# Performance work log

Hardware: AMD Instinct MI355X
Metric: run time of the kernel (lower is better)

## Reference

```python
import jax, jax.numpy as jnp
import numpy as np

V, D, H, L, B, S = 8192, 128, 8, 2, 1, 128
HD = D // H
HID = int(8 * D / 3)
EPS = 1e-6


def setup_inputs() -> dict:
    key = jax.random.key(0)
    ks = jax.random.split(key, 12)
    sc = 0.02
    return {
        "idx": jax.random.randint(ks[0], (B, S), 0, V),
        "w_raw": jax.random.normal(ks[1], (D, V), jnp.float32) * sc,
        "norm1_w": jnp.ones((L, D), jnp.float32),
        "norm2_w": jnp.ones((L, D), jnp.float32),
        "wq": jax.random.normal(ks[2], (L, D, D), jnp.float32) * sc,
        "wk": jax.random.normal(ks[3], (L, D, D), jnp.float32) * sc,
        "wv": jax.random.normal(ks[4], (L, D, D), jnp.float32) * sc,
        "wo": jax.random.normal(ks[5], (L, D, D), jnp.float32) * sc,
        "w1": jax.random.normal(ks[6], (L, D, HID), jnp.float32) * sc,
        "w3": jax.random.normal(ks[7], (L, D, HID), jnp.float32) * sc,
        "w2": jax.random.normal(ks[8], (L, HID, D), jnp.float32) * sc,
        "final_norm_w": jnp.ones((D,), jnp.float32),
    }


def rmsnorm(x, w):
    return x * jax.lax.rsqrt(jnp.mean(x * x, axis=-1, keepdims=True) + EPS) * w


def rope_cos_sin(seqlen, hd):
    inv = 1.0 / (10000.0 ** (jnp.arange(0, hd, 2, dtype=jnp.float32) / hd))
    t = jnp.arange(seqlen, dtype=jnp.float32)
    f = jnp.outer(t, inv)  # (S, hd/2)
    return jnp.cos(f), jnp.sin(f)


def apply_rope(x, cos, sin):
    # x: (B,S,H,HD); interleaved complex pairs as in Llama
    x0, x1 = x[..., 0::2], x[..., 1::2]
    c = cos[None, :, None, :]
    s = sin[None, :, None, :]
    r0 = x0 * c - x1 * s
    r1 = x0 * s + x1 * c
    return jnp.stack([r0, r1], axis=-1).reshape(x.shape)


def forward(idx, w_raw, norm1_w, norm2_w, wq, wk, wv, wo, w1, w2, w3, final_norm_w):
    Wemb = jax.nn.sigmoid(w_raw)                 # (D,V)
    x = Wemb.T[idx]                              # Yoneda one-hot @ W.T == gather -> (B,S,D)
    cos, sin = rope_cos_sin(S, HD)
    causal = jnp.tril(jnp.ones((S, S), bool))[None, None]  # (1,1,S,S)
    scale = 1.0 / jnp.sqrt(jnp.float32(HD))
    for i in range(L):
        # Multi-Universe attention (heads == universes), RoPE, causal SDPA
        h = rmsnorm(x, norm1_w[i])
        q = (h @ wq[i]).reshape(B, S, H, HD)
        k = (h @ wk[i]).reshape(B, S, H, HD)
        v = (h @ wv[i]).reshape(B, S, H, HD)
        q = apply_rope(q, cos, sin)
        k = apply_rope(k, cos, sin)
        scores = jnp.einsum("bihd,bjhd->bhij", q, k) * scale
        scores = jnp.where(causal, scores, jnp.float32(-1e9))
        attn = jax.nn.softmax(scores, axis=-1)
        o = jnp.einsum("bhij,bjhd->bihd", attn, v).reshape(B, S, D) @ wo[i]
        x = x + o
        # SwiGLU FFN
        h2 = rmsnorm(x, norm2_w[i])
        x = x + (jax.nn.silu(h2 @ w1[i]) * (h2 @ w3[i])) @ w2[i]
    x_norm = rmsnorm(x, final_norm_w)
    # Godel-Heyting reachability head
    x_n = x_norm / jnp.linalg.norm(x_norm, axis=-1, keepdims=True)      # (B,S,D)
    v_n = (Wemb / jnp.linalg.norm(Wemb, axis=0, keepdims=True)).T        # (V,D)
    a = x_n[:, :, None, :]                                               # (B,S,1,D)
    b = v_n[None, None, :, :]                                            # (1,1,V,D)
    # strict Godel implication: a => b = 1 if a <= b else b
    imp = jnp.where(a <= b, jnp.float32(1.0), b)                         # (B,S,V,D)
    logits = jnp.clip(imp.mean(axis=-1), 1e-6, 1.0 - 1e-6)               # (B,S,V)
    return logits


def reference(idx, w_raw, norm1_w, norm2_w, wq, wk, wv, wo, w1, w2, w3, final_norm_w):
    return forward(idx, w_raw, norm1_w, norm2_w, wq, wk, wv, wo, w1, w2, w3, final_norm_w)
```

## Files before the change

### kernel.cpp

```cpp
#include <hip/hip_runtime.h>
#include <math.h>

#define V 8192
#define D 128
#define NH 8
#define HD 16
#define SEQ 128
#define HID 341
#define EPS 1e-6f

__device__ __forceinline__ float sigm(float x) { return 1.0f / (1.0f + __expf(-x)); }

__device__ __forceinline__ float block_sum256(float v, float* scratch) {
    #pragma unroll
    for (int m = 32; m > 0; m >>= 1) v += __shfl_xor(v, m);
    if ((threadIdx.x & 63) == 0) scratch[threadIdx.x >> 6] = v;
    __syncthreads();
    float s = (scratch[0] + scratch[1]) + (scratch[2] + scratch[3]);
    __syncthreads();
    return s;
}

__device__ __forceinline__ float block_sum512(float v, float* scratch) {
    #pragma unroll
    for (int m = 32; m > 0; m >>= 1) v += __shfl_xor(v, m);
    if ((threadIdx.x & 63) == 0) scratch[threadIdx.x >> 6] = v;
    __syncthreads();
    float s = ((scratch[0] + scratch[1]) + (scratch[2] + scratch[3])) +
              ((scratch[4] + scratch[5]) + (scratch[6] + scratch[7]));
    __syncthreads();
    return s;
}

__global__ __launch_bounds__(256, 1) void k_embed_qkv(
    const int* __restrict__ idx, const float* __restrict__ w_raw,
    const float* __restrict__ wq, const float* __restrict__ wk,
    const float* __restrict__ wv, const float* __restrict__ n1w,
    const float* __restrict__ w1, const float* __restrict__ w3,
    const float* __restrict__ w2, const float* __restrict__ wo,
    float* __restrict__ x, float* __restrict__ q, float* __restrict__ k,
    float* __restrict__ v, float* __restrict__ sink) {
    int t = threadIdx.x;
    if (blockIdx.x >= SEQ) {
        int g = (blockIdx.x - SEQ) * 256 + t;
        float acc = 0.f;
        const float4* p = (const float4*)w_raw;
        for (int i = g; i < 262144; i += 65536) {
            float4 u = p[i];
            acc += u.x + u.y + u.z + u.w;
        }
        p = (const float4*)w1;
        if (g < 21824) { float4 u = p[g]; acc += u.x + u.y + u.z + u.w; }
        p = (const float4*)w3;
        if (g < 21824) { float4 u = p[g]; acc += u.x + u.y + u.z + u.w; }
        p = (const float4*)w2;
        if (g < 21824) { float4 u = p[g]; acc += u.x + u.y + u.z + u.w; }
        p = (const float4*)wq;
        if (g < 8192) { float4 u = p[g]; acc += u.x + u.y + u.z + u.w; }
        p = (const float4*)wk;
        if (g < 8192) { float4 u = p[g]; acc += u.x + u.y + u.z + u.w; }
        p = (const float4*)wv;
        if (g < 8192) { float4 u = p[g]; acc += u.x + u.y + u.z + u.w; }
        p = (const float4*)wo;
        if (g < 8192) { float4 u = p[g]; acc += u.x + u.y + u.z + u.w; }
        if (acc == 1234.5678f) sink[0] = acc;
        return;
    }
    __shared__ float hr[D], qrow[D], krow[D], vpart[2][D], scr[4];
    int s = blockIdx.x;
    int col = t & 127, half = t >> 7, dlo = half * 64;
    float xv = 0.f;
    if (t < 128) xv = sigm(w_raw[t * V + idx[s]]);
    float wpre[128];
    const float* wsel = (t < 128) ? wq : wk;
    #pragma unroll
    for (int d = 0; d < 128; ++d) wpre[d] = wsel[d * D + col];
    float wvpre[64];
    #pragma unroll
    for (int d = 0; d < 64; ++d) wvpre[d] = wv[(dlo + d) * D + col];
    if (t < 128) x[s * D + t] = xv;
    float ss = block_sum256(xv * xv, scr);
    float r = 1.0f / sqrtf(ss * (1.0f / D) + EPS);
    if (t < 128) hr[t] = xv * r * n1w[t];
    __syncthreads();
    float a0 = 0, a1 = 0, a2 = 0, a3 = 0;
    #pragma unroll
    for (int d = 0; d < 128; d += 4) {
        a0 += hr[d] * wpre[d];
        a1 += hr[d + 1] * wpre[d + 1];
        a2 += hr[d + 2] * wpre[d + 2];
        a3 += hr[d + 3] * wpre[d + 3];
    }
    float qk = (a0 + a1) + (a2 + a3);
    float b0 = 0, b1 = 0, b2 = 0, b3 = 0;
    #pragma unroll
    for (int d = 0; d < 64; d += 4) {
        b0 += hr[dlo + d] * wvpre[d];
        b1 += hr[dlo + d + 1] * wvpre[d + 1];
        b2 += hr[dlo + d + 2] * wvpre[d + 2];
        b3 += hr[dlo + d + 3] * wvpre[d + 3];
    }
    vpart[half][col] = (b0 + b1) + (b2 + b3);
    if (t < 128) qrow[col] = qk;
    else krow[col] = qk;
    __syncthreads();
    if (t < 128) {
        v[s * D + t] = vpart[0][t] + vpart[1][t];
        int c = t & (HD - 1);
        int m = c >> 1;
        float fr = (float)s * expf(-(float)m * 1.15129254649702283e+00f);
        float cs = cosf(fr), sn = sinf(fr);
        int base = t & ~1;
        float qe = qrow[base], qod = qrow[base + 1];
        float ke = krow[base], kod = krow[base + 1];
        q[s * D + t] = (c & 1) ? (qe * sn + qod * cs) : (qe * cs - qod * sn);
        k[s * D + t] = (c & 1) ? (ke * sn + kod * cs) : (ke * cs - kod * sn);
    }
}

template <int MODE>
__global__ __launch_bounds__(512, 2) void k_layer(
    const float* __restrict__ q, const float* __restrict__ kg,
    const float* __restrict__ vg, float* __restrict__ x,
    const float* __restrict__ wo, const float* __restrict__ n2w,
    const float* __restrict__ w1, const float* __restrict__ w3,
    const float* __restrict__ w2, const float* __restrict__ wq,
    const float* __restrict__ wk, const float* __restrict__ wv,
    const float* __restrict__ n1w, float* __restrict__ qo, float* __restrict__ ko,
    float* __restrict__ vo, const float* __restrict__ fw, float* __restrict__ xng) {
    __shared__ float ps[NH][SEQ + 1];
    __shared__ float qs[D], orow[D], h2[D];
    __shared__ float part[4][D];
    __shared__ float afA[HID], afB[HID], af[HID];
    __shared__ float rl[NH];
    __shared__ float scr[8];
    int s = blockIdx.x, t = threadIdx.x;
    int col = t & 127, quarter = t >> 7;
    int jlo = quarter * 32, dlo = quarter * 32;

    float qv = 0.f, xr = 0.f;
    if (t < 128) {
        qv = q[s * D + t];
        xr = x[s * D + t];
    }
    float4 kp[2][4];
    #pragma unroll
    for (int u = 0; u < 2; ++u) {
        const float4* p = (const float4*)&kg[col * D + (quarter + 4 * u) * HD];
        kp[u][0] = p[0]; kp[u][1] = p[1]; kp[u][2] = p[2]; kp[u][3] = p[3];
    }
    float vpre[32];
    #pragma unroll
    for (int j = 0; j < 32; ++j) vpre[j] = vg[(jlo + j) * D + col];
    float wopre[32];
    #pragma unroll
    for (int u = 0; u < 32; ++u) wopre[u] = wo[(dlo + u) * D + col];

    if (t < 128) qs[t] = qv;
    __syncthreads();

    #pragma unroll
    for (int u = 0; u < 2; ++u) {
        int h = quarter + 4 * u;
        const float* qh = &qs[h * HD];
        float acc = kp[u][0].x * qh[0] + kp[u][0].y * qh[1] + kp[u][0].z * qh[2] +
                    kp[u][0].w * qh[3] + kp[u][1].x * qh[4] + kp[u][1].y * qh[5] +
                    kp[u][1].z * qh[6] + kp[u][1].w * qh[7] + kp[u][2].x * qh[8] +
                    kp[u][2].y * qh[9] + kp[u][2].z * qh[10] + kp[u][2].w * qh[11] +
                    kp[u][3].x * qh[12] + kp[u][3].y * qh[13] + kp[u][3].z * qh[14] +
                    kp[u][3].w * qh[15];
        ps[h][col] = (col <= s) ? acc * 0.25f : 0.f;
    }
    __syncthreads();

    {
        int h = t >> 6, lane = t & 63;
        float pm = -1e30f;
        for (int j = lane; j <= s; j += 64) pm = fmaxf(pm, ps[h][j]);
        #pragma unroll
        for (int m = 32; m > 0; m >>= 1) pm = fmaxf(pm, __shfl_xor(pm, m));
        float psum = 0.f;
        for (int j = lane; j <= s; j += 64) {
            float e = __expf(ps[h][j] - pm);
            ps[h][j] = e;
            psum += e;
        }
        #pragma unroll
        for (int m = 32; m > 0; m >>= 1) psum += __shfl_xor(psum, m);
        if (lane == 0) rl[h] = 1.0f / psum;
    }
    __syncthreads();

    {
        int h = col >> 4;
        float a0 = 0, a1 = 0, a2 = 0, a3 = 0;
        #pragma unroll
        for (int j = 0; j < 32; j += 4) {
            a0 += ps[h][jlo + j] * vpre[j];
            a1 += ps[h][jlo + j + 1] * vpre[j + 1];
            a2 += ps[h][jlo + j + 2] * vpre[j + 2];
            a3 += ps[h][jlo + j + 3] * vpre[j + 3];
        }
        part[quarter][col] = (a0 + a1) + (a2 + a3);
    }
    __syncthreads();
    if (t < 128) orow[t] = ((part[0][t] + part[1][t]) + (part[2][t] + part[3][t])) * rl[t >> 4];
    __syncthreads();

    {
        float a0 = 0, a1 = 0;
        #pragma unroll
        for (int u = 0; u < 32; u += 2) {
            a0 += orow[dlo + u] * wopre[u];
            a1 += orow[dlo + u + 1] * wopre[u + 1];
        }
        part[quarter][col] = a0 + a1;
    }
    __syncthreads();
    float xn = 0.f;
    if (t < 128) xn = xr + (part[0][t] + part[1][t]) + (part[2][t] + part[3][t]);
    float ss2 = block_sum512((t < 128) ? xn * xn : 0.f, scr);
    float r2 = 1.0f / sqrtf(ss2 * (1.0f / D) + EPS);
    if (t < 128) h2[t] = xn * r2 * n2w[t];
    __syncthreads();

    for (int task = t; task < 2 * HID; task += 512) {
        int mat = task >= HID;
        int c2 = mat ? (task - HID) : task;
        const float* w = mat ? w3 : w1;
        float a0 = 0, a1 = 0, a2 = 0, a3 = 0;
        #pragma unroll 8
        for (int d = 0; d < D; d += 4) {
            a0 += h2[d] * w[d * HID + c2];
            a1 += h2[d + 1] * w[(d + 1) * HID + c2];
            a2 += h2[d + 2] * w[(d + 2) * HID + c2];
            a3 += h2[d + 3] * w[(d + 3) * HID + c2];
        }
        if (mat) afB[c2] = (a0 + a1) + (a2 + a3);
        else afA[c2] = (a0 + a1) + (a2 + a3);
    }
    __syncthreads();
    if (t < HID) {
        float a1v = afA[t];
        af[t] = (a1v / (1.0f + __expf(-a1v))) * afB[t];
    }
    __syncthreads();

    {
        int lo = quarter * 85;
        int hi = (quarter == 3) ? 341 : lo + 85;
        float a0 = 0, a1 = 0, a2 = 0, a3 = 0;
        int tt = lo;
        #pragma unroll 8
        for (; tt + 3 < hi; tt += 4) {
            a0 += af[tt] * w2[tt * D + col];
            a1 += af[tt + 1] * w2[(tt + 1) * D + col];
            a2 += af[tt + 2] * w2[(tt + 2) * D + col];
            a3 += af[tt + 3] * w2[(tt + 3) * D + col];
        }
        for (; tt < hi; ++tt) a0 += af[tt] * w2[tt * D + col];
        part[quarter][col] = (a0 + a1) + (a2 + a3);
    }
    __syncthreads();
    float x2 = 0.f;
    if (t < 128) {
        x2 = xn + (part[0][t] + part[1][t]) + (part[2][t] + part[3][t]);
        if (MODE == 0) x[s * D + t] = x2;
    }

    float ss = block_sum512((t < 128) ? x2 * x2 : 0.f, scr);
    float r = 1.0f / sqrtf(ss * (1.0f / D) + EPS);

    if constexpr (MODE == 0) {
        if (t < 128) h2[t] = x2 * r * n1w[t];
        __syncthreads();
        float qk = 0.f;
        if (quarter < 3) {
            const float* wsel = (quarter == 0) ? wq : ((quarter == 1) ? wk : wv);
            float a0 = 0, a1 = 0, a2 = 0, a3 = 0;
            #pragma unroll 8
            for (int d = 0; d < D; d += 4) {
                a0 += h2[d] * wsel[d * D + col];
                a1 += h2[d + 1] * wsel[(d + 1) * D + col];
                a2 += h2[d + 2] * wsel[(d + 2) * D + col];
                a3 += h2[d + 3] * wsel[(d + 3) * D + col];
            }
            qk = (a0 + a1) + (a2 + a3);
        }
        if (quarter == 0) qs[col] = qk;
        else if (quarter == 1) orow[col] = qk;
        else if (quarter == 2) part[0][col] = qk;
        __syncthreads();
        if (t < 128) {
            vo[s * D + t] = part[0][t];
            int c = t & (HD - 1);
            int mm = c >> 1;
            float fr = (float)s * expf(-(float)mm * 1.15129254649702283e+00f);
            float cs = cosf(fr), sn = sinf(fr);
            int base = t & ~1;
            float qe = qs[base], qod = qs[base + 1];
            float ke = orow[base], kod = orow[base + 1];
            qo[s * D + t] = (c & 1) ? (qe * sn + qod * cs) : (qe * cs - qod * sn);
            ko[s * D + t] = (c & 1) ? (ke * sn + kod * cs) : (ke * cs - kod * sn);
        }
    } else {
        float y = (t < 128) ? x2 * r * fw[t] : 0.f;
        float nn = block_sum512(y * y, scr);
        if (t < 128) xng[t * SEQ + s] = y / sqrtf(nn);
    }
}

__global__ __launch_bounds__(256) void k_logits(const float* __restrict__ xng,
                                                const float* __restrict__ w_raw,
                                                float* __restrict__ out) {
    __shared__ float xs[D * 64];
    __shared__ float vs[D * 32];
    __shared__ float nred[256];
    __shared__ float invn_s[32];
    int t = threadIdx.x;
    int sbase = (blockIdx.x & 1) * 64;
    int vbase = (blockIdx.x >> 1) * 32;
    for (int i = t; i < D * 64; i += 256) {
        int d = i >> 6, s2 = i & 63;
        xs[i] = xng[d * SEQ + sbase + s2];
    }
    for (int i = t; i < D * 32; i += 256) {
        int d = i >> 5, jj = i & 31;
        vs[i] = sigm(w_raw[d * V + vbase + jj]);
    }
    __syncthreads();
    {
        int colc = t & 31, dp = t >> 5;
        float p = 0.f;
        for (int u = 0; u < 16; ++u) {
            float vv = vs[(dp * 16 + u) * 32 + colc];
            p += vv * vv;
        }
        nred[t] = p;
    }
    __syncthreads();
    if (t < 32) {
        float sum = 0.f;
        for (int u = 0; u < 8; ++u) sum += nred[u * 32 + t];
        invn_s[t] = 1.0f / sqrtf(sum);
    }
    __syncthreads();
    for (int i = t; i < D * 32; i += 256) vs[i] *= invn_s[i & 31];
    __syncthreads();
    int vg = t & 15;
    int sg = t >> 4;
    float acc[4][2] = {};
    for (int d = 0; d < D; ++d) {
        float4 xq = *(const float4*)&xs[d * 64 + sg * 4];
        float2 vq = *(const float2*)&vs[d * 32 + vg * 2];
        acc[0][0] += (xq.x <= vq.x) ? 1.0f : vq.x;
        acc[0][1] += (xq.x <= vq.y) ? 1.0f : vq.y;
        acc[1][0] += (xq.y <= vq.x) ? 1.0f : vq.x;
        acc[1][1] += (xq.y <= vq.y) ? 1.0f : vq.y;
        acc[2][0] += (xq.z <= vq.x) ? 1.0f : vq.x;
        acc[2][1] += (xq.z <= vq.y) ? 1.0f : vq.y;
        acc[3][0] += (xq.w <= vq.x) ? 1.0f : vq.x;
        acc[3][1] += (xq.w <= vq.y) ? 1.0f : vq.y;
    }
    const float inv128 = 1.0f / 128.0f;
    #pragma unroll
    for (int si = 0; si < 4; ++si) {
        int s = sbase + sg * 4 + si;
        float2 ov;
        ov.x = fminf(fmaxf(acc[si][0] * inv128, 1e-6f), 1.0f - 1e-6f);
        ov.y = fminf(fmaxf(acc[si][1] * inv128, 1e-6f), 1.0f - 1e-6f);
        *(float2*)&out[s * V + vbase + vg * 2] = ov;
    }
}

extern "C" void kernel_launch(void* const* d_in, const int* in_sizes, int n_in,
                              void* d_out, int out_size, void* d_ws, size_t ws_size,
                              hipStream_t stream) {
    const int* idx = (const int*)d_in[0];
    const float* w_raw = (const float*)d_in[1];
    const float* n1w = (const float*)d_in[2];
    const float* n2w = (const float*)d_in[3];
    const float* wq = (const float*)d_in[4];
    const float* wk = (const float*)d_in[5];
    const float* wv = (const float*)d_in[6];
    const float* wo = (const float*)d_in[7];
    const float* w1 = (const float*)d_in[8];
    const float* w3 = (const float*)d_in[9];
    const float* w2 = (const float*)d_in[10];
    const float* fnw = (const float*)d_in[11];
    float* out = (float*)d_out;
    float* ws = (float*)d_ws;

    float* x    = ws;
    float* q1   = ws + 16384;
    float* k1   = ws + 32768;
    float* v1   = ws + 49152;
    float* q2   = ws + 65536;
    float* k2   = ws + 81920;
    float* v2   = ws + 98304;
    float* xng  = ws + 114688;
    float* sink = ws + 131072;

    k_embed_qkv<<<dim3(SEQ + 256), dim3(256), 0, stream>>>(
        idx, w_raw, wq, wk, wv, n1w, w1, w3, w2, wo, x, q1, k1, v1, sink);
    k_layer<0><<<dim3(SEQ), dim3(512), 0, stream>>>(
        q1, k1, v1, x, wo, n2w, w1, w3, w2,
        wq + D * D, wk + D * D, wv + D * D, n1w + D, q2, k2, v2,
        (const float*)nullptr, (float*)nullptr);
    k_layer<1><<<dim3(SEQ), dim3(512), 0, stream>>>(
        q2, k2, v2, x, wo + D * D, n2w + D, w1 + D * HID, w3 + D * HID,
        w2 + HID * D, (const float*)nullptr, (const float*)nullptr,
        (const float*)nullptr, (const float*)nullptr, (float*)nullptr,
        (float*)nullptr, (float*)nullptr, fnw, xng);
    k_logits<<<dim3(512), dim3(256), 0, stream>>>(xng, w_raw, out);
}
```

Baseline: 141.5 us.

## Widen per-token layer kernel to 1024 threads and drop register prefetch

Doubles the k_layer block from 512 to 1024 threads, so each 128-thread group handles 16 rows instead of 32 for the attention value, output projection and w2 reductions, and one head per group for QK scores. The register prefetch arrays for K, V and Wo are removed; those loads now happen inline inside the loops. The w1/w3 projection becomes a single pass with one task per thread. This aims to cut per-thread serial work and register pressure in a 128-block launch that leaves most CUs idle, at the cost of more partial-sum reduction and of no longer issuing the global loads early.

```diff
diff --git a/kernel.cpp b/kernel.cpp
--- a/kernel.cpp
+++ b/kernel.cpp
@@ -21,13 +21,15 @@
     return s;
 }
 
-__device__ __forceinline__ float block_sum512(float v, float* scratch) {
+__device__ __forceinline__ float block_sum1024(float v, float* scratch) {
     #pragma unroll
     for (int m = 32; m > 0; m >>= 1) v += __shfl_xor(v, m);
     if ((threadIdx.x & 63) == 0) scratch[threadIdx.x >> 6] = v;
     __syncthreads();
     float s = ((scratch[0] + scratch[1]) + (scratch[2] + scratch[3])) +
-              ((scratch[4] + scratch[5]) + (scratch[6] + scratch[7]));
+              ((scratch[4] + scratch[5]) + (scratch[6] + scratch[7])) +
+              ((scratch[8] + scratch[9]) + (scratch[10] + scratch[11])) +
+              ((scratch[12] + scratch[13]) + (scratch[14] + scratch[15]));
     __syncthreads();
     return s;
 }
@@ -119,7 +121,7 @@
 }
 
 template <int MODE>
-__global__ __launch_bounds__(512, 2) void k_layer(
+__global__ __launch_bounds__(1024, 4) void k_layer(
     const float* __restrict__ q, const float* __restrict__ kg,
     const float* __restrict__ vg, float* __restrict__ x,
     const float* __restrict__ wo, const float* __restrict__ n2w,
@@ -130,50 +132,35 @@
     float* __restrict__ vo, const float* __restrict__ fw, float* __restrict__ xng) {
     __shared__ float ps[NH][SEQ + 1];
     __shared__ float qs[D], orow[D], h2[D];
-    __shared__ float part[4][D];
+    __shared__ float part[8][D];
     __shared__ float afA[HID], afB[HID], af[HID];
     __shared__ float rl[NH];
-    __shared__ float scr[8];
+    __shared__ float scr[16];
     int s = blockIdx.x, t = threadIdx.x;
-    int col = t & 127, quarter = t >> 7;
-    int jlo = quarter * 32, dlo = quarter * 32;
+    int col = t & 127, g8 = t >> 7;
+    int jlo = g8 * 16, dlo = g8 * 16;
 
     float qv = 0.f, xr = 0.f;
     if (t < 128) {
         qv = q[s * D + t];
         xr = x[s * D + t];
-    }
-    float4 kp[2][4];
-    #pragma unroll
-    for (int u = 0; u < 2; ++u) {
-        const float4* p = (const float4*)&kg[col * D + (quarter + 4 * u) * HD];
-        kp[u][0] = p[0]; kp[u][1] = p[1]; kp[u][2] = p[2]; kp[u][3] = p[3];
-    }
-    float vpre[32];
-    #pragma unroll
-    for (int j = 0; j < 32; ++j) vpre[j] = vg[(jlo + j) * D + col];
-    float wopre[32];
-    #pragma unroll
-    for (int u = 0; u < 32; ++u) wopre[u] = wo[(dlo + u) * D + col];
-
-    if (t < 128) qs[t] = qv;
-    __syncthreads();
-
-    #pragma unroll
-    for (int u = 0; u < 2; ++u) {
-        int h = quarter + 4 * u;
-        const float* qh = &qs[h * HD];
-        float acc = kp[u][0].x * qh[0] + kp[u][0].y * qh[1] + kp[u][0].z * qh[2] +
-                    kp[u][0].w * qh[3] + kp[u][1].x * qh[4] + kp[u][1].y * qh[5] +
-                    kp[u][1].z * qh[6] + kp[u][1].w * qh[7] + kp[u][2].x * qh[8] +
-                    kp[u][2].y * qh[9] + kp[u][2].z * qh[10] + kp[u][2].w * qh[11] +
-                    kp[u][3].x * qh[12] + kp[u][3].y * qh[13] + kp[u][3].z * qh[14] +
-                    kp[u][3].w * qh[15];
-        ps[h][col] = (col <= s) ? acc * 0.25f : 0.f;
+        qs[t] = qv;
     }
     __syncthreads();
 
     {
+        const float4* kp = (const float4*)&kg[col * D + g8 * HD];
+        float4 k0 = kp[0], k1v = kp[1], k2v = kp[2], k3v = kp[3];
+        const float* qh = &qs[g8 * HD];
+        float acc = k0.x * qh[0] + k0.y * qh[1] + k0.z * qh[2] + k0.w * qh[3] +
+                    k1v.x * qh[4] + k1v.y * qh[5] + k1v.z * qh[6] + k1v.w * qh[7] +
+                    k2v.x * qh[8] + k2v.y * qh[9] + k2v.z * qh[10] + k2v.w * qh[11] +
+                    k3v.x * qh[12] + k3v.y * qh[13] + k3v.z * qh[14] + k3v.w * qh[15];
+        ps[g8][col] = (col <= s) ? acc * 0.25f : 0.f;
+    }
+    __syncthreads();
+
+    if (t < 512) {
         int h = t >> 6, lane = t & 63;
         float pm = -1e30f;
         for (int j = lane; j <= s; j += 64) pm = fmaxf(pm, ps[h][j]);
@@ -195,38 +182,42 @@
         int h = col >> 4;
         float a0 = 0, a1 = 0, a2 = 0, a3 = 0;
         #pragma unroll
-        for (int j = 0; j < 32; j += 4) {
-            a0 += ps[h][jlo + j] * vpre[j];
-            a1 += ps[h][jlo + j + 1] * vpre[j + 1];
-            a2 += ps[h][jlo + j + 2] * vpre[j + 2];
-            a3 += ps[h][jlo + j + 3] * vpre[j + 3];
-        }
-        part[quarter][col] = (a0 + a1) + (a2 + a3);
-    }
-    __syncthreads();
-    if (t < 128) orow[t] = ((part[0][t] + part[1][t]) + (part[2][t] + part[3][t])) * rl[t >> 4];
+        for (int j = 0; j < 16; j += 4) {
+            a0 += ps[h][jlo + j] * vg[(jlo + j) * D + col];
+            a1 += ps[h][jlo + j + 1] * vg[(jlo + j + 1) * D + col];
+            a2 += ps[h][jlo + j + 2] * vg[(jlo + j + 2) * D + col];
+            a3 += ps[h][jlo + j + 3] * vg[(jlo + j + 3) * D + col];
+        }
+        part[g8][col] = (a0 + a1) + (a2 + a3);
+    }
+    __syncthreads();
+    if (t < 128)
+        orow[t] = (((part[0][t] + part[1][t]) + (part[2][t] + part[3][t])) +
+                   ((part[4][t] + part[5][t]) + (part[6][t] + part[7][t]))) * rl[t >> 4];
     __syncthreads();
 
     {
         float a0 = 0, a1 = 0;
         #pragma unroll
-        for (int u = 0; u < 32; u += 2) {
-            a0 += orow[dlo + u] * wopre[u];
-            a1 += orow[dlo + u + 1] * wopre[u + 1];
-        }
-        part[quarter][col] = a0 + a1;
+        for (int u = 0; u < 16; u += 2) {
+            a0 += orow[dlo + u] * wo[(dlo + u) * D + col];
+            a1 += orow[dlo + u + 1] * wo[(dlo + u + 1) * D + col];
+        }
+        part[g8][col] = a0 + a1;
     }
     __syncthreads();
     float xn = 0.f;
-    if (t < 128) xn = xr + (part[0][t] + part[1][t]) + (part[2][t] + part[3][t]);
-    float ss2 = block_sum512((t < 128) ? xn * xn : 0.f, scr);
+    if (t < 128)
+        xn = xr + ((part[0][t] + part[1][t]) + (part[2][t] + part[3][t])) +
+             ((part[4][t] + part[5][t]) + (part[6][t] + part[7][t]));
+    float ss2 = block_sum1024((t < 128) ? xn * xn : 0.f, scr);
     float r2 = 1.0f / sqrtf(ss2 * (1.0f / D) + EPS);
     if (t < 128) h2[t] = xn * r2 * n2w[t];
     __syncthreads();
 
-    for (int task = t; task < 2 * HID; task += 512) {
-        int mat = task >= HID;
-        int c2 = mat ? (task - HID) : task;
+    if (t < 2 * HID) {
+        int mat = t >= HID;
+        int c2 = mat ? (t - HID) : t;
         const float* w = mat ? w3 : w1;
         float a0 = 0, a1 = 0, a2 = 0, a3 = 0;
         #pragma unroll 8
@@ -247,8 +238,8 @@
     __syncthreads();
 
     {
-        int lo = quarter * 85;
-        int hi = (quarter == 3) ? 341 : lo + 85;
+        int lo = g8 * 43;
+        int hi = (lo + 43 > HID) ? HID : lo + 43;
         float a0 = 0, a1 = 0, a2 = 0, a3 = 0;
         int tt = lo;
         #pragma unroll 8
@@ -259,24 +250,25 @@
             a3 += af[tt + 3] * w2[(tt + 3) * D + col];
         }
         for (; tt < hi; ++tt) a0 += af[tt] * w2[tt * D + col];
-        part[quarter][col] = (a0 + a1) + (a2 + a3);
+        part[g8][col] = (a0 + a1) + (a2 + a3);
     }
     __syncthreads();
     float x2 = 0.f;
     if (t < 128) {
-        x2 = xn + (part[0][t] + part[1][t]) + (part[2][t] + part[3][t]);
+        x2 = xn + ((part[0][t] + part[1][t]) + (part[2][t] + part[3][t])) +
+             ((part[4][t] + part[5][t]) + (part[6][t] + part[7][t]));
         if (MODE == 0) x[s * D + t] = x2;
     }
 
-    float ss = block_sum512((t < 128) ? x2 * x2 : 0.f, scr);
+    float ss = block_sum1024((t < 128) ? x2 * x2 : 0.f, scr);
     float r = 1.0f / sqrtf(ss * (1.0f / D) + EPS);
 
     if constexpr (MODE == 0) {
         if (t < 128) h2[t] = x2 * r * n1w[t];
         __syncthreads();
         float qk = 0.f;
-        if (quarter < 3) {
-            const float* wsel = (quarter == 0) ? wq : ((quarter == 1) ? wk : wv);
+        if (g8 < 3) {
+            const float* wsel = (g8 == 0) ? wq : ((g8 == 1) ? wk : wv);
             float a0 = 0, a1 = 0, a2 = 0, a3 = 0;
             #pragma unroll 8
             for (int d = 0; d < D; d += 4) {
@@ -287,9 +279,9 @@
             }
             qk = (a0 + a1) + (a2 + a3);
         }
-        if (quarter == 0) qs[col] = qk;
-        else if (quarter == 1) orow[col] = qk;
-        else if (quarter == 2) part[0][col] = qk;
+        if (g8 == 0) qs[col] = qk;
+        else if (g8 == 1) orow[col] = qk;
+        else if (g8 == 2) part[0][col] = qk;
         __syncthreads();
         if (t < 128) {
             vo[s * D + t] = part[0][t];
@@ -305,7 +297,7 @@
         }
     } else {
         float y = (t < 128) ? x2 * r * fw[t] : 0.f;
-        float nn = block_sum512(y * y, scr);
+        float nn = block_sum1024(y * y, scr);
         if (t < 128) xng[t * SEQ + s] = y / sqrtf(nn);
     }
 }
@@ -403,11 +395,11 @@
 
     k_embed_qkv<<<dim3(SEQ + 256), dim3(256), 0, stream>>>(
         idx, w_raw, wq, wk, wv, n1w, w1, w3, w2, wo, x, q1, k1, v1, sink);
-    k_layer<0><<<dim3(SEQ), dim3(512), 0, stream>>>(
+    k_layer<0><<<dim3(SEQ), dim3(1024), 0, stream>>>(
         q1, k1, v1, x, wo, n2w, w1, w3, w2,
         wq + D * D, wk + D * D, wv + D * D, n1w + D, q2, k2, v2,
         (const float*)nullptr, (float*)nullptr);
-    k_layer<1><<<dim3(SEQ), dim3(512), 0, stream>>>(
+    k_layer<1><<<dim3(SEQ), dim3(1024), 0, stream>>>(
         q2, k2, v2, x, wo + D * D, n2w + D, w1 + D * HID, w3 + D * HID,
         w2 + HID * D, (const float*)nullptr, (const float*)nullptr,
         (const float*)nullptr, (const float*)nullptr, (float*)nullptr,
```

New measurement: 139.5 us (median of 2 runs). About the same (-1.4%).
